# Optimization experiments

Hardware: AMD Instinct MI355X
Metric: run time of the kernel (lower is better)

The kernel has to match this reference:

```python
import jax, jax.numpy as jnp
import numpy as np
import math

NHID = 32
FEAT_SIZE = 32
FEAT_SIZE_LIST = [16, 32, 32, 32]
SEQ_LEN = len(FEAT_SIZE_LIST)   # 4
N_EDGE_LABELS = 3
NLAYERS = 2
N_GRAPHS = 64
FINAL = SEQ_LEN * NHID          # 128


def _pos_enc(max_len, dim):
    pe = np.zeros((max_len, dim), dtype=np.float32)
    pos = np.arange(max_len, dtype=np.float32)[:, None]
    div = np.exp(np.arange(0, dim, 2, dtype=np.float32) * (-math.log(10000.0) / dim))
    pe[:, 0::2] = np.sin(pos * div)
    pe[:, 1::2] = np.cos(pos * div)
    return jnp.asarray(pe)


def _feature_attention(x, wqkv, w1, b1, w2, b2):
    # x: [N, S*NHID] -> attention over the S feature 'tokens' per node
    N, D = x.shape
    S = D // NHID
    xr = x.reshape(N, S, NHID)
    qkv = jnp.einsum('nsf,fh->nsh', xr, wqkv)          # [N,S,3*NHID]
    q, k, v = jnp.split(qkv, 3, axis=-1)
    att = jax.nn.softmax(jnp.einsum('nsh,nth->nst', q, k) / jnp.sqrt(jnp.asarray(NHID, x.dtype)), axis=-1)
    y = jnp.einsum('nst,nth->nsh', att, v)             # [N,S,NHID]
    y = y + (jax.nn.relu(y @ w1 + b1) @ w2 + b2)       # residual FFN
    return y.reshape(N, -1)


def setup_inputs() -> dict:
    key = jax.random.key(0)
    ks = jax.random.split(key, 16)
    N = 100000
    E = 800000
    inp = {
        'x': jax.random.normal(ks[0], (N, 112), dtype=jnp.float32),
        'edge_index0': jax.random.randint(ks[1], (2, E), 0, N),
        'edge_index1': jax.random.randint(ks[2], (2, E), 0, N),
        'edge_index2': jax.random.randint(ks[3], (2, E), 0, N),
        'batch': jnp.sort(jax.random.randint(ks[4], (N,), 0, N_GRAPHS)),
    }
    s = 0.05
    # FeatureLinear encoder (bias-free)
    inp['W_emb'] = jax.random.normal(ks[5], (FEAT_SIZE, NHID), dtype=jnp.float32) * s
    # Per layer: [root, conv0, conv1, conv2] FeatureAttention params, stacked
    A = 1 + N_EDGE_LABELS
    inp['qkv'] = jax.random.normal(ks[6], (NLAYERS, A, NHID, 3 * NHID), dtype=jnp.float32) * s
    inp['ffn_w1'] = jax.random.normal(ks[7], (NLAYERS, A, NHID, NHID), dtype=jnp.float32) * s
    inp['ffn_b1'] = jnp.zeros((NLAYERS, A, NHID), dtype=jnp.float32)
    inp['ffn_w2'] = jax.random.normal(ks[8], (NLAYERS, A, NHID, NHID), dtype=jnp.float32) * s
    inp['ffn_b2'] = jnp.zeros((NLAYERS, A, NHID), dtype=jnp.float32)
    # Heuristic decoder MLP: 128 -> 128 -> 1
    inp['mlp_w1'] = jax.random.normal(ks[9], (FINAL, FINAL), dtype=jnp.float32) * s
    inp['mlp_b1'] = jnp.zeros((FINAL,), dtype=jnp.float32)
    inp['mlp_w2'] = jax.random.normal(ks[10], (FINAL, 1), dtype=jnp.float32) * s
    inp['mlp_b2'] = jnp.zeros((1,), dtype=jnp.float32)
    return inp


def reference(x, edge_index0, edge_index1, edge_index2, batch,
              W_emb, qkv, ffn_w1, ffn_b1, ffn_w2, ffn_b2,
              mlp_w1, mlp_b1, mlp_w2, mlp_b2):
    N = x.shape[0]
    edge_indices = [edge_index0, edge_index1, edge_index2]

    # padding: split by feat_size_list, right-pad each chunk to FEAT_SIZE
    offs = np.cumsum(FEAT_SIZE_LIST)[:-1].tolist()
    chunks = jnp.split(x, offs, axis=1)
    padded = [jnp.pad(c, ((0, 0), (0, FEAT_SIZE - c.shape[1]))) for c in chunks]
    h = jnp.concatenate(padded, axis=1)                       # [N, SEQ_LEN*FEAT_SIZE]

    # sinusoidal positional encoding over the SEQ_LEN feature tokens
    pe = _pos_enc(10, FEAT_SIZE)[:SEQ_LEN]                    # [SEQ_LEN, FEAT_SIZE]
    h = (h.reshape(N, SEQ_LEN, FEAT_SIZE) + pe[None]).reshape(N, -1)

    # FeatureLinear encoder: per-token linear FEAT_SIZE -> NHID
    h = jnp.einsum('nsf,fh->nsh', h.reshape(N, SEQ_LEN, FEAT_SIZE), W_emb).reshape(N, -1)

    # RGNN layers: root attention + per-edge-label attention->scatter-sum
    for l in range(NLAYERS):
        x_out = _feature_attention(h, qkv[l, 0], ffn_w1[l, 0], ffn_b1[l, 0], ffn_w2[l, 0], ffn_b2[l, 0])
        for e in range(N_EDGE_LABELS):
            a = e + 1
            xt = _feature_attention(h, qkv[l, a], ffn_w1[l, a], ffn_b1[l, a], ffn_w2[l, a], ffn_b2[l, a])
            src, dst = edge_indices[e][0], edge_indices[e][1]
            x_out = x_out + jax.ops.segment_sum(xt[src], dst, num_segments=N)
        h = jax.nn.relu(x_out)

    # global mean pool over graphs
    sums = jax.ops.segment_sum(h, batch, num_segments=N_GRAPHS)
    cnts = jax.ops.segment_sum(jnp.ones((N,), h.dtype), batch, num_segments=N_GRAPHS)
    g = sums / jnp.maximum(cnts, 1.0)[:, None]                # [G, FINAL]

    # heuristic decoder
    out = jax.nn.relu(g @ mlp_w1 + mlp_b1) @ mlp_w2 + mlp_b2  # [G, 1]
    return out.squeeze(1)                                     # [G]
```

## Files before the change

### kernel.cpp

```cpp
#include <hip/hip_runtime.h>
#include <hip/hip_bf16.h>
#include <cstdint>
#include <cstddef>


typedef __attribute__((ext_vector_type(8))) short bf16x8;
typedef __attribute__((ext_vector_type(4))) float f32x4;
typedef __attribute__((ext_vector_type(2))) float f32x2;

#if defined(__has_builtin)
#if __has_builtin(__builtin_amdgcn_cvt_pk_fp8_f32) && __has_builtin(__builtin_amdgcn_cvt_pk_f32_fp8)
#define HW_FP8 1
#endif
#if __has_builtin(__builtin_amdgcn_cvt_pk_bf16_f32)
#define HW_PKBF16 1
#endif
#endif

__device__ inline short f2bf(float f) {
    union { float f; unsigned u; } v; v.f = f;
    unsigned r = (v.u + 0x7FFFu + ((v.u >> 16) & 1u)) >> 16;
    return (short)r;
}
__device__ inline float bf2f(unsigned short b) {
    union { unsigned u; float f; } v; v.u = ((unsigned)b) << 16;
    return v.f;
}
#ifdef HW_PKBF16
typedef __attribute__((ext_vector_type(2))) __bf16 bf16x2_t;
__device__ inline unsigned pk2(float a, float b) {
    union { bf16x2_t v; unsigned u; } c;
    c.v = __builtin_amdgcn_cvt_pk_bf16_f32(a, b);
    return c.u;
}
#else
__device__ inline unsigned pk2(float a, float b) {
    unsigned ua = __float_as_uint(a) + 0x8000u;
    unsigned ub = __float_as_uint(b) + 0x8000u;
    return __builtin_amdgcn_perm(ub, ua, 0x07060302u);
}
#endif

#ifndef HW_FP8
__device__ inline unsigned char f2fp8_sw(float f) {
    unsigned s = (__float_as_uint(f) >> 31) & 1u;
    float a = fminf(fabsf(f), 448.f);
    unsigned char bits;
    if (a < 0.015625f) {
        bits = (unsigned char)__float2int_rn(a * 512.f);
    } else {
        int e; float m = frexpf(a, &e);
        int mf = __float2int_rn(m * 16.f);
        if (mf == 16) { mf = 8; e += 1; }
        int ef = e - 1 + 7;
        if (ef > 15) { ef = 15; mf = 14; }
        bits = (unsigned char)((ef << 3) | (mf & 7));
    }
    return (unsigned char)((s << 7) | bits);
}
__device__ inline float fp82f_sw(unsigned b) {
    int s = (b >> 7) & 1, e = (b >> 3) & 15, m = b & 7;
    float v = e ? ldexpf((float)(8 + m), e - 10) : ldexpf((float)m, -9);
    return s ? -v : v;
}
#endif

__device__ inline unsigned pk4fp8(float v0, float v1, float v2, float v3) {
#ifdef HW_FP8
    int w = __builtin_amdgcn_cvt_pk_fp8_f32(v0, v1, 0, false);
    w = __builtin_amdgcn_cvt_pk_fp8_f32(v2, v3, w, true);
    return (unsigned)w;
#else
    return (unsigned)f2fp8_sw(v0) | ((unsigned)f2fp8_sw(v1) << 8) |
           ((unsigned)f2fp8_sw(v2) << 16) | ((unsigned)f2fp8_sw(v3) << 24);
#endif
}
__device__ inline float2 up2fp8(unsigned short raw) {
#ifdef HW_FP8
    f32x2 f = __builtin_amdgcn_cvt_pk_f32_fp8((int)(unsigned)raw, false);
    return make_float2(f[0], f[1]);
#else
    return make_float2(fp82f_sw(raw & 0xffu), fp82f_sw((raw >> 8) & 0xffu));
#endif
}

__device__ inline void acc8(float* a, uint2 v) {
#ifdef HW_FP8
    f32x2 f0 = __builtin_amdgcn_cvt_pk_f32_fp8((int)v.x, false);
    f32x2 f1 = __builtin_amdgcn_cvt_pk_f32_fp8((int)v.x, true);
    f32x2 f2 = __builtin_amdgcn_cvt_pk_f32_fp8((int)v.y, false);
    f32x2 f3 = __builtin_amdgcn_cvt_pk_f32_fp8((int)v.y, true);
    a[0] += f0[0]; a[1] += f0[1]; a[2] += f1[0]; a[3] += f1[1];
    a[4] += f2[0]; a[5] += f2[1]; a[6] += f3[0]; a[7] += f3[1];
#else
    unsigned b0 = v.x, b1 = v.y;
#pragma unroll
    for (int j = 0; j < 4; ++j) a[j]     += fp82f_sw((b0 >> (8 * j)) & 0xffu);
#pragma unroll
    for (int j = 0; j < 4; ++j) a[4 + j] += fp82f_sw((b1 >> (8 * j)) & 0xffu);
#endif
}
__device__ inline void acc16(float* a, uint4 v) {
    acc8(a,     make_uint2(v.x, v.y));
    acc8(a + 8, make_uint2(v.z, v.w));
}

__global__ __launch_bounds__(64) void wprep_kernel(
    const float* __restrict__ qkv, const float* __restrict__ fw1,
    const float* __restrict__ fw2, const float* __restrict__ Wemb,
    unsigned short* __restrict__ wpack, float* __restrict__ pwc,
    unsigned char* __restrict__ xtzr,
    int* __restrict__ bcnt, int* __restrict__ gres,
    float* __restrict__ gsum, float* __restrict__ gcnt)
{
    const int pi = blockIdx.x;
    const int lane = threadIdx.x;
    const int gid = pi * 64 + lane;
    for (int i = gid; i < 256; i += 512) { bcnt[i] = 0; gres[i] = 0; }
    for (int i = gid; i < 64 * 128; i += 512) gsum[i] = 0.f;
    if (gid < 64) gcnt[gid] = 0.f;
    if (gid < 32) ((int*)xtzr)[gid] = 0;

    const int q = lane >> 4, m = lane & 15;
    const float* Wq = qkv + (size_t)pi * 32 * 96;
    const float* W1 = fw1 + (size_t)pi * 32 * 32;
    const float* W2 = fw2 + (size_t)pi * 32 * 32;
    unsigned short* dst = wpack + (size_t)pi * 10 * 64 * 8;
#pragma unroll
    for (int ci = 0; ci < 6; ++ci)
#pragma unroll
        for (int j = 0; j < 8; ++j)
            dst[(ci * 64 + lane) * 8 + j] =
                (unsigned short)f2bf(Wq[(q * 8 + j) * 96 + ci * 16 + m]);
#pragma unroll
    for (int t = 0; t < 2; ++t)
#pragma unroll
        for (int j = 0; j < 8; ++j) {
            dst[((6 + t) * 64 + lane) * 8 + j] =
                (unsigned short)f2bf(W1[(q * 8 + j) * 32 + t * 16 + m]);
            dst[((8 + t) * 64 + lane) * 8 + j] =
                (unsigned short)f2bf(W2[(q * 8 + j) * 32 + t * 16 + m]);
        }

    if (pi == 0) {
        const int c = lane & 31;
        for (int ts = lane >> 5; ts < 4; ts += 2) {
            float accp = 0.f;
            for (int f = 0; f < 32; ++f) {
                float div = __expf(-(float)(f & ~1) * (logf(10000.0f) / 32.0f));
                float ang = (float)ts * div;
                float pv = (f & 1) ? cosf(ang) : sinf(ang);
                accp += pv * Wemb[f * 32 + c];
            }
            pwc[ts * 32 + c] = accp;
        }
    }
}

__global__ __launch_bounds__(256) void enc_kernel(
    const float* __restrict__ x, const float* __restrict__ Wemb,
    const float* __restrict__ pwc, unsigned short* __restrict__ h, int N)
{
    __shared__ float sx[64 * 116];
    const int t = threadIdx.x;
    const int nbase = blockIdx.x * 64;

    {
        const float4* xg = (const float4*)x;
        const size_t g4base = ((size_t)nbase * 112) >> 2;
        const size_t lim4 = ((size_t)N * 112) >> 2;
#pragma unroll
        for (int rep = 0; rep < 7; ++rep) {
            int i = t + rep * 256;
            float4 v = make_float4(0.f, 0.f, 0.f, 0.f);
            if (g4base + (size_t)i < lim4) v = xg[g4base + i];
            int row = i / 28;
            int col4 = i - row * 28;
            *(float4*)&sx[row * 116 + col4 * 4] = v;
        }
    }
    __syncthreads();

    const int nl = t >> 2, ts = t & 3;
    const int node = nbase + nl;
    const int offs_[4] = {0, 16, 48, 80};
    const int nv_[4] = {4, 8, 8, 8};
    const int off = offs_[ts];
    const int nv = nv_[ts];

    float xr[32];
#pragma unroll
    for (int j = 0; j < 8; ++j) {
        float4 v = make_float4(0.f, 0.f, 0.f, 0.f);
        if (j < nv) v = *(const float4*)&sx[nl * 116 + off + 4 * j];
        *(float4*)&xr[4 * j] = v;
    }

    float acc[32];
    {
        const float4* pw4 = (const float4*)(pwc + ts * 32);
#pragma unroll
        for (int j = 0; j < 8; ++j) *(float4*)&acc[4 * j] = pw4[j];
    }

#pragma unroll
    for (int f = 0; f < 32; ++f) {
        float xv = xr[f];
#pragma unroll
        for (int c = 0; c < 32; ++c)
            acc[c] = fmaf(xv, Wemb[f * 32 + c], acc[c]);
    }

    if (node < N) {
        unsigned rp[16];
#pragma unroll
        for (int j = 0; j < 16; ++j) rp[j] = pk2(acc[2 * j], acc[2 * j + 1]);
        unsigned short* hp = h + (size_t)node * 128 + ts * 32;
#pragma unroll
        for (int j = 0; j < 4; ++j)
            ((uint4*)hp)[j] = make_uint4(rp[4 * j], rp[4 * j + 1],
                                         rp[4 * j + 2], rp[4 * j + 3]);
    }
}

#define ATT_WAVES 4
#define WLDS 5376

__global__ __launch_bounds__(256, 3) void attn4_kernel(
    const unsigned short* __restrict__ in,
    unsigned short* __restrict__ outR, unsigned char* __restrict__ out3,
    const unsigned short* __restrict__ wpack,
    const float* __restrict__ fb1, const float* __restrict__ fb2,
    int pibase, int N)
{
    __shared__ char smem[ATT_WAVES * 2 * WLDS];
    const int lane = threadIdx.x & 63;
    const int wave = threadIdx.x >> 6;
    const int q = lane >> 4;
    const int m = lane & 15;

    char* wb0 = smem + wave * (2 * WLDS);

#pragma unroll
    for (int u = 0; u < 2; ++u) {
        int* p32 = (int*)(wb0 + u * WLDS + 4096);
        for (int i = lane; i < 320; i += 64) p32[i] = 0;
    }

    const f32x4 zf = {0.f, 0.f, 0.f, 0.f};
    const int pi = pibase + wave;
    unsigned char* out8 = out3 + (size_t)(wave - 1) * N * 128;

    bf16x8 wqkv[6], w1f[2], w2f[2];
    float b1r[2][4], b2r[2][4];
    {
        const unsigned short* wp = wpack + ((size_t)pi * 10 * 64 + lane) * 8;
#pragma unroll
        for (int ci = 0; ci < 6; ++ci)
            wqkv[ci] = *(const bf16x8*)(wp + ci * 64 * 8);
#pragma unroll
        for (int t = 0; t < 2; ++t) {
            w1f[t] = *(const bf16x8*)(wp + (6 + t) * 64 * 8);
            w2f[t] = *(const bf16x8*)(wp + (8 + t) * 64 * 8);
#pragma unroll
            for (int r = 0; r < 4; ++r) {
                b1r[t][r] = fb1[pi * 32 + 16 * t + q * 4 + r];
                b2r[t][r] = fb2[pi * 32 + 16 * t + q * 4 + r];
            }
        }
    }

    const int nsuper = (N + 7) >> 3;
    for (int stile = blockIdx.x; stile < nsuper; stile += gridDim.x) {
        const int n0 = stile * 8;

        bf16x8 ax[2];
#pragma unroll
        for (int u = 0; u < 2; ++u) {
            bf16x8 a = {0, 0, 0, 0, 0, 0, 0, 0};
            int nm = n0 + 4 * u + (m >> 2);
            if (nm < N)
                a = *(const bf16x8*)(in + (size_t)(n0 + 4 * u) * 128 + m * 32 + q * 8);
            ax[u] = a;
        }

#pragma unroll
        for (int u = 0; u < 2; ++u) {
            char* wbu = wb0 + u * WLDS;
            short* Qb = (short*)(wbu);
            short* Kb = (short*)(wbu + 1280);
            short* VT = (short*)(wbu + 2560);
            short* Pb = (short*)(wbu + 4096);

            f32x4 aQ[2], aK[2], aV[2];
#pragma unroll
            for (int t = 0; t < 2; ++t) {
                aQ[t] = __builtin_amdgcn_mfma_f32_16x16x32_bf16(wqkv[t],     ax[u], zf, 0, 0, 0);
                aK[t] = __builtin_amdgcn_mfma_f32_16x16x32_bf16(wqkv[2 + t], ax[u], zf, 0, 0, 0);
                aV[t] = __builtin_amdgcn_mfma_f32_16x16x32_bf16(ax[u], wqkv[4 + t], zf, 0, 0, 0);
            }
#pragma unroll
            for (int t = 0; t < 2; ++t) {
                uint2 dq, dk, dv;
                dq.x = pk2(aQ[t][0], aQ[t][1]); dq.y = pk2(aQ[t][2], aQ[t][3]);
                dk.x = pk2(aK[t][0], aK[t][1]); dk.y = pk2(aK[t][2], aK[t][3]);
                dv.x = pk2(aV[t][0], aV[t][1]); dv.y = pk2(aV[t][2], aV[t][3]);
                *(uint2*)(Qb + m * 40 + 16 * t + q * 4) = dq;
                *(uint2*)(Kb + m * 40 + 16 * t + q * 4) = dk;
                *(uint2*)(VT + (16 * t + m) * 24 + q * 4) = dv;
            }

            bf16x8 aKf = *(const bf16x8*)(Kb + m * 40 + q * 8);
            bf16x8 bQf = *(const bf16x8*)(Qb + m * 40 + q * 8);
            f32x4 st = __builtin_amdgcn_mfma_f32_16x16x32_bf16(aKf, bQf, zf, 0, 0, 0);

            float v0 = st[0] * 0.1767766952966369f;
            float v1 = st[1] * 0.1767766952966369f;
            float v2 = st[2] * 0.1767766952966369f;
            float v3 = st[3] * 0.1767766952966369f;
            float mx = fmaxf(fmaxf(v0, v1), fmaxf(v2, v3));
            float e0 = __expf(v0 - mx), e1 = __expf(v1 - mx);
            float e2 = __expf(v2 - mx), e3 = __expf(v3 - mx);
            float inv = 1.0f / (e0 + e1 + e2 + e3);
            if (q == (m >> 2)) {
                uint2 dp;
                dp.x = pk2(e0 * inv, e1 * inv);
                dp.y = pk2(e2 * inv, e3 * inv);
                *(uint2*)(Pb + m * 40 + q * 4) = dp;
            }

            f32x4 y[2];
#pragma unroll
            for (int t = 0; t < 2; ++t) {
                bf16x8 aVf = {0, 0, 0, 0, 0, 0, 0, 0};
                bf16x8 bPf = {0, 0, 0, 0, 0, 0, 0, 0};
                if (q < 2) {
                    aVf = *(const bf16x8*)(VT + (16 * t + m) * 24 + q * 8);
                    bPf = *(const bf16x8*)(Pb + m * 40 + q * 8);
                }
                y[t] = __builtin_amdgcn_mfma_f32_16x16x32_bf16(aVf, bPf, zf, 0, 0, 0);
            }
#pragma unroll
            for (int t = 0; t < 2; ++t) {
                uint2 dy;
                dy.x = pk2(y[t][0], y[t][1]); dy.y = pk2(y[t][2], y[t][3]);
                *(uint2*)(Qb + m * 40 + 16 * t + q * 4) = dy;
            }

            bf16x8 bY = *(const bf16x8*)(Qb + m * 40 + q * 8);
            f32x4 z1[2];
#pragma unroll
            for (int t = 0; t < 2; ++t)
                z1[t] = __builtin_amdgcn_mfma_f32_16x16x32_bf16(w1f[t], bY, zf, 0, 0, 0);
#pragma unroll
            for (int t = 0; t < 2; ++t) {
                uint2 dz;
                dz.x = pk2(fmaxf(z1[t][0] + b1r[t][0], 0.f),
                           fmaxf(z1[t][1] + b1r[t][1], 0.f));
                dz.y = pk2(fmaxf(z1[t][2] + b1r[t][2], 0.f),
                           fmaxf(z1[t][3] + b1r[t][3], 0.f));
                *(uint2*)(Kb + m * 40 + 16 * t + q * 4) = dz;
            }

            bf16x8 bZ = *(const bf16x8*)(Kb + m * 40 + q * 8);
            f32x4 o[2];
#pragma unroll
            for (int t = 0; t < 2; ++t)
                o[t] = __builtin_amdgcn_mfma_f32_16x16x32_bf16(w2f[t], bZ, zf, 0, 0, 0);

            if (n0 + 4 * u + (m >> 2) < N) {
                if (wave == 0) {
#pragma unroll
                    for (int t = 0; t < 2; ++t) {
                        uint2 dd;
                        dd.x = pk2(y[t][0] + o[t][0] + b2r[t][0],
                                   y[t][1] + o[t][1] + b2r[t][1]);
                        dd.y = pk2(y[t][2] + o[t][2] + b2r[t][2],
                                   y[t][3] + o[t][3] + b2r[t][3]);
                        *(uint2*)(outR + (size_t)(n0 + 4 * u) * 128 + m * 32 + 16 * t + q * 4) = dd;
                    }
                } else {
#pragma unroll
                    for (int t = 0; t < 2; ++t) {
                        unsigned pw8 = pk4fp8(
                            (y[t][0] + o[t][0] + b2r[t][0]) * 16.f,
                            (y[t][1] + o[t][1] + b2r[t][1]) * 16.f,
                            (y[t][2] + o[t][2] + b2r[t][2]) * 16.f,
                            (y[t][3] + o[t][3] + b2r[t][3]) * 16.f);
                        *(unsigned*)(out8 + (size_t)(n0 + 4 * u) * 128 + m * 32 + 16 * t + q * 4) = pw8;
                    }
                }
            }
        }
    }
}

#define PA_CHUNK 4096
#define PA_SHIFT 9
#define PA_MAXB  256
#define HB_K     16

__global__ __launch_bounds__(256) void histB_kernel(
    const int* __restrict__ e0, const int* __restrict__ e1,
    const int* __restrict__ e2, int* __restrict__ bcnt, int E)
{
    __shared__ int lh[PA_MAXB];
    const int lab = blockIdx.y;
    const int* e = (lab == 0) ? e0 : (lab == 1) ? e1 : e2;
    const int t = threadIdx.x;
    for (int i = t; i < PA_MAXB; i += 256) lh[i] = 0;
    __syncthreads();
    const int base = blockIdx.x * 256 * HB_K;
#pragma unroll
    for (int k = 0; k < HB_K; ++k) {
        int i = base + k * 256 + t;
        if (i < E) atomicAdd(&lh[e[E + i] >> PA_SHIFT], 1);
    }
    __syncthreads();
    for (int i = t; i < PA_MAXB; i += 256)
        if (lh[i]) atomicAdd(&bcnt[i], lh[i]);
}

__global__ __launch_bounds__(256) void bscan_kernel(
    const int* __restrict__ bcnt, int* __restrict__ bbase)
{
    __shared__ int sd[PA_MAXB];
    const int t = threadIdx.x;
    sd[t] = bcnt[t];
    __syncthreads();
    int own = sd[t];
    for (int o = 1; o < 256; o <<= 1) {
        int v = (t >= o) ? sd[t - o] : 0;
        __syncthreads();
        sd[t] += v;
        __syncthreads();
    }
    bbase[t] = sd[t] - own;
}

__global__ __launch_bounds__(256) void placeA_kernel(
    const int* __restrict__ e0, const int* __restrict__ e1, const int* __restrict__ e2,
    const int* __restrict__ bbase, int* __restrict__ gres,
    int2* __restrict__ pairs, int E, int N)
{
    __shared__ int2 sStage[PA_CHUNK];
    __shared__ int sCnt[PA_MAXB], sScan[PA_MAXB], sCur[PA_MAXB], sGB[PA_MAXB];

    const int lab = blockIdx.y;
    const int t = threadIdx.x;
    const int base = blockIdx.x * PA_CHUNK;
    const int* e = (lab == 0) ? e0 : (lab == 1) ? e1 : e2;
    const int srcoff = lab * N;
    const int nbins = (N + (1 << PA_SHIFT) - 1) >> PA_SHIFT;

    for (int i = t; i < PA_MAXB; i += 256) { sCnt[i] = 0; sCur[i] = 0; }
    __syncthreads();

    int msrc[16], mdst[16];
    const int cnt_total = min(PA_CHUNK, E - base);
#pragma unroll
    for (int k = 0; k < 16; ++k) {
        int i = base + k * 256 + t;
        if (i < E) {
            msrc[k] = srcoff + e[i];
            int d = e[E + i];
            mdst[k] = d;
            atomicAdd(&sCnt[d >> PA_SHIFT], 1);
        } else mdst[k] = -1;
    }
    __syncthreads();

    sScan[t] = sCnt[t];
    __syncthreads();
    for (int o = 1; o < 256; o <<= 1) {
        int v = (t >= o) ? sScan[t - o] : 0;
        __syncthreads();
        sScan[t] += v;
        __syncthreads();
    }
    if (t < nbins && sCnt[t] > 0)
        sGB[t] = bbase[t] + atomicAdd(&gres[t], sCnt[t]);
    __syncthreads();

#pragma unroll
    for (int k = 0; k < 16; ++k) {
        if (mdst[k] >= 0) {
            int bin = mdst[k] >> PA_SHIFT;
            int r = atomicAdd(&sCur[bin], 1);
            sStage[(sScan[bin] - sCnt[bin]) + r] = make_int2(msrc[k], mdst[k]);
        }
    }
    __syncthreads();

    for (int i = t; i < cnt_total; i += 256) {
        int2 pr = sStage[i];
        int bin = pr.y >> PA_SHIFT;
        pairs[sGB[bin] + (i - (sScan[bin] - sCnt[bin]))] = pr;
    }
}

__global__ __launch_bounds__(512) void placeB_kernel(
    const int2* __restrict__ pairs, const int* __restrict__ bbase,
    const int* __restrict__ bcnt, int* __restrict__ offs,
    int* __restrict__ csr, int N, int nbins)
{
    __shared__ int sCnt[512], sScan[512], sFill[512];
    const int bin = blockIdx.x;
    const int t = threadIdx.x;
    const int n0 = bin << PA_SHIFT;
    const int n1 = min(n0 + 512, N);
    const int len = n1 - n0;
    const int rb  = bbase[bin];
    const int cnt = bcnt[bin];
    const int2* gp = pairs + rb;

    sCnt[t] = 0; sFill[t] = 0;
    __syncthreads();
    for (int i = t; i < cnt; i += 512)
        atomicAdd(&sCnt[gp[i].y - n0], 1);
    __syncthreads();
    sScan[t] = sCnt[t];
    __syncthreads();
    for (int o = 1; o < 512; o <<= 1) {
        int v = (t >= o) ? sScan[t - o] : 0;
        __syncthreads();
        sScan[t] += v;
        __syncthreads();
    }
    const int excl = sScan[t] - sCnt[t];
    if (t < len) offs[n0 + t] = rb + excl;
    if (bin == nbins - 1 && t == 0) offs[N] = rb + cnt;
    sScan[t] = excl;
    __syncthreads();

    for (int i = t; i < cnt; i += 512) {
        int2 pr = gp[i];
        int ln = pr.y - n0;
        int p = atomicAdd(&sFill[ln], 1);
        csr[rb + sScan[ln] + p] = pr.x;
    }
}

__global__ __launch_bounds__(256) void agg3_kernel(
    const unsigned short* __restrict__ xtR,
    const unsigned char* __restrict__ xt3,
    const int* __restrict__ csr, const int* __restrict__ offs,
    unsigned short* __restrict__ hout, int N)
{
    const int wv = threadIdx.x >> 6, lane = threadIdx.x & 63;
    const int oct = lane >> 3;
    const int fl  = lane & 7;
    const int dst = blockIdx.x * 32 + wv * 8 + oct;
    const int ZR  = 3 * N;
    const unsigned fb = (unsigned)fl << 4;

    const int beg = offs[min(dst, N)];
    const int end = offs[min(dst + 1, N)];
    const int last = end - 1;

    const unsigned short* rp = xtR + (size_t)min(dst, N - 1) * 128 + fl * 16;
    bf16x8 rv0 = *(const bf16x8*)(rp);
    bf16x8 rv1 = *(const bf16x8*)(rp + 8);

    float a[16];
#pragma unroll
    for (int i = 0; i < 16; ++i) a[i] = 0.f;

    int k = beg;
    int i0 = csr[k];
    int i1 = csr[k + 1];
    int c0 = (k     > last) ? ZR : i0;
    int c1 = (k + 1 > last) ? ZR : i1;

    while (__any(k < end)) {
        uint4 v0 = *(const uint4*)(xt3 + (((unsigned)c0) << 7) + fb);
        uint4 v1 = *(const uint4*)(xt3 + (((unsigned)c1) << 7) + fb);
        int k2 = min(k + 2, end);
        int j0 = csr[k2];
        int j1 = csr[k2 + 1];
        c0 = (k2     > last) ? ZR : j0;
        c1 = (k2 + 1 > last) ? ZR : j1;
        acc16(a, v0);
        acc16(a, v1);
        k = k2;
    }

    if (dst < N) {
        unsigned r[8];
#pragma unroll
        for (int t = 0; t < 4; ++t) {
            float f0 = bf2f((unsigned short)rv0[2 * t])     + 0.0625f * a[2 * t];
            float f1 = bf2f((unsigned short)rv0[2 * t + 1]) + 0.0625f * a[2 * t + 1];
            r[t] = pk2(fmaxf(f0, 0.f), fmaxf(f1, 0.f));
        }
#pragma unroll
        for (int t = 0; t < 4; ++t) {
            float f0 = bf2f((unsigned short)rv1[2 * t])     + 0.0625f * a[8 + 2 * t];
            float f1 = bf2f((unsigned short)rv1[2 * t + 1]) + 0.0625f * a[8 + 2 * t + 1];
            r[4 + t] = pk2(fmaxf(f0, 0.f), fmaxf(f1, 0.f));
        }
        unsigned short* hp = hout + (size_t)dst * 128 + fl * 16;
        *(uint4*)hp       = make_uint4(r[0], r[1], r[2], r[3]);
        *(uint4*)(hp + 8) = make_uint4(r[4], r[5], r[6], r[7]);
    }
}

__global__ __launch_bounds__(256) void pool_kernel(
    const unsigned short* __restrict__ in, const int* __restrict__ batch,
    float* __restrict__ gsum, float* __restrict__ gcnt, int N)
{
    int t = threadIdx.x;
    int j = t & 127, half = t >> 7;
    int n0 = blockIdx.x * 64 + half * 32;
    float acc = 0.f, c = 0.f; int cur = -1;
    for (int i = 0; i < 32; ++i) {
        int n = n0 + i;
        if (n >= N) break;
        int g = batch[n];
        if (g != cur) {
            if (cur >= 0) {
                atomicAdd(&gsum[cur * 128 + j], acc);
                if (j == 0) atomicAdd(&gcnt[cur], c);
            }
            cur = g; acc = 0.f; c = 0.f;
        }
        acc += bf2f(in[(size_t)n * 128 + j]);
        c += 1.f;
    }
    if (cur >= 0) {
        atomicAdd(&gsum[cur * 128 + j], acc);
        if (j == 0) atomicAdd(&gcnt[cur], c);
    }
}

__global__ __launch_bounds__(128) void dec_kernel(
    const float* __restrict__ gsum, const float* __restrict__ gcnt,
    const float* __restrict__ W1, const float* __restrict__ B1,
    const float* __restrict__ W2, const float* __restrict__ B2,
    float* __restrict__ out)
{
    __shared__ float sg[128];
    __shared__ float sh[128];
    int t = threadIdx.x, b = blockIdx.x;
    float cinv = 1.0f / fmaxf(gcnt[b], 1.0f);
    sg[t] = gsum[b * 128 + t] * cinv;
    __syncthreads();
    float acc = B1[t];
    for (int f = 0; f < 128; ++f) acc += sg[f] * W1[f * 128 + t];
    sh[t] = fmaxf(acc, 0.f) * W2[t];
    __syncthreads();
    for (int o = 64; o > 0; o >>= 1) {
        if (t < o) sh[t] += sh[t + o];
        __syncthreads();
    }
    if (t == 0) out[b] = sh[0] + B2[0];
}

extern "C" void kernel_launch(void* const* d_in, const int* in_sizes, int n_in,
                              void* d_out, int out_size, void* d_ws, size_t ws_size,
                              hipStream_t stream)
{
    const float* x    = (const float*)d_in[0];
    const int*   e0   = (const int*)d_in[1];
    const int*   e1   = (const int*)d_in[2];
    const int*   e2   = (const int*)d_in[3];
    const int*   bat  = (const int*)d_in[4];
    const float* Wemb = (const float*)d_in[5];
    const float* qkv  = (const float*)d_in[6];
    const float* fw1  = (const float*)d_in[7];
    const float* fb1  = (const float*)d_in[8];
    const float* fw2  = (const float*)d_in[9];
    const float* fb2  = (const float*)d_in[10];
    const float* mw1  = (const float*)d_in[11];
    const float* mb1  = (const float*)d_in[12];
    const float* mw2  = (const float*)d_in[13];
    const float* mb2  = (const float*)d_in[14];
    const int N = in_sizes[0] / 112;
    const int E = in_sizes[1] / 2;
    float* outp = (float*)d_out;
    (void)n_in; (void)out_size; (void)ws_size;

    char* w = (char*)d_ws;
    auto alloc = [&](size_t bytes) {
        char* p = w; w += (bytes + 255) & ~(size_t)255; return p;
    };
    unsigned short* h0    = (unsigned short*)alloc((size_t)N * 128 * 2);
    unsigned short* h1    = (unsigned short*)alloc((size_t)N * 128 * 2);
    unsigned short* xtR   = (unsigned short*)alloc((size_t)N * 128 * 2);
    unsigned char*  xt3   = (unsigned char*)alloc((size_t)3 * N * 128 + 128);
    unsigned short* wpack = (unsigned short*)alloc(8 * 10 * 64 * 8 * 2);
    float* pwc   = (float*)alloc(128 * 4);
    int*   csr   = (int*)alloc((size_t)3 * E * 4 + 64);
    int*   offs  = (int*)alloc((size_t)(N + 1) * 4);
    int*   bcnt  = (int*)alloc(PA_MAXB * 4);
    int*   bbase = (int*)alloc(PA_MAXB * 4);
    int*   gres  = (int*)alloc(PA_MAXB * 4);
    float* gsum  = (float*)alloc(64 * 128 * 4);
    float* gcnt  = (float*)alloc(64 * 4);
    int2* pairs = (int2*)xtR;
    unsigned char* xtzr = xt3 + (size_t)3 * N * 128;

    const int nbins = (N + (1 << PA_SHIFT) - 1) >> PA_SHIFT;

    wprep_kernel<<<8, 64, 0, stream>>>(qkv, fw1, fw2, Wemb, wpack, pwc, xtzr,
                                       bcnt, gres, gsum, gcnt);
    enc_kernel<<<(N + 63) / 64, 256, 0, stream>>>(x, Wemb, pwc, h0, N);

    histB_kernel<<<dim3((E + 256 * HB_K - 1) / (256 * HB_K), 3), 256, 0, stream>>>(
        e0, e1, e2, bcnt, E);
    bscan_kernel<<<1, 256, 0, stream>>>(bcnt, bbase);
    placeA_kernel<<<dim3((E + PA_CHUNK - 1) / PA_CHUNK, 3), 256, 0, stream>>>(
        e0, e1, e2, bbase, gres, pairs, E, N);
    placeB_kernel<<<nbins, 512, 0, stream>>>(pairs, bbase, bcnt, offs, csr, N, nbins);

    const int ATT_GRID = 768;
    auto run_layer = [&](const unsigned short* lin, unsigned short* lout, int l) {
        attn4_kernel<<<ATT_GRID, 256, 0, stream>>>(
            lin, xtR, xt3, wpack, fb1, fb2, l * 4, N);
        agg3_kernel<<<(N + 31) / 32, 256, 0, stream>>>(xtR, xt3, csr, offs, lout, N);
    };
    run_layer(h0, h1, 0);
    run_layer(h1, h0, 1);

    pool_kernel<<<(N + 63) / 64, 256, 0, stream>>>(h0, bat, gsum, gcnt, N);
    dec_kernel<<<64, 128, 0, stream>>>(gsum, gcnt, mw1, mb1, mw2, mb2, outp);
}
```

Measured before the change: 465.7 us.

## Share attention P buffer across sub-tiles and unroll gather loop by four

The attention kernel now keeps a single per-wave P-scratch region for both sub-tiles, which cuts per-block LDS use. It raises the launch-bounds occupancy hint from 3 to 4 blocks and the persistent grid from 768 to 1024. The aggregation kernel gathers four neighbor rows per iteration instead of two, putting more loads in flight to hide gather latency. Sharing P across sub-tiles adds a possible ordering hazard if the two sub-tiles overlap, and the extra loads raise register pressure. The csr prefetch also reads up to three entries past the current index, which relies on padding past the end of the array.

```diff
diff --git a/kernel.cpp b/kernel.cpp
--- a/kernel.cpp
+++ b/kernel.cpp
@@ -224,26 +224,27 @@
 }
 
 #define ATT_WAVES 4
-#define WLDS 5376
-
-__global__ __launch_bounds__(256, 3) void attn4_kernel(
+#define ULDS 4096
+#define WLDS_W (2 * ULDS + 1280)
+
+__global__ __launch_bounds__(256, 4) void attn4_kernel(
     const unsigned short* __restrict__ in,
     unsigned short* __restrict__ outR, unsigned char* __restrict__ out3,
     const unsigned short* __restrict__ wpack,
     const float* __restrict__ fb1, const float* __restrict__ fb2,
     int pibase, int N)
 {
-    __shared__ char smem[ATT_WAVES * 2 * WLDS];
+    __shared__ char smem[ATT_WAVES * WLDS_W];
     const int lane = threadIdx.x & 63;
     const int wave = threadIdx.x >> 6;
     const int q = lane >> 4;
     const int m = lane & 15;
 
-    char* wb0 = smem + wave * (2 * WLDS);
-
-#pragma unroll
-    for (int u = 0; u < 2; ++u) {
-        int* p32 = (int*)(wb0 + u * WLDS + 4096);
+    char* wb0 = smem + wave * WLDS_W;
+    short* Pb = (short*)(wb0 + 2 * ULDS);
+
+    {
+        int* p32 = (int*)Pb;
         for (int i = lane; i < 320; i += 64) p32[i] = 0;
     }
 
@@ -286,11 +287,10 @@
 
 #pragma unroll
         for (int u = 0; u < 2; ++u) {
-            char* wbu = wb0 + u * WLDS;
+            char* wbu = wb0 + u * ULDS;
             short* Qb = (short*)(wbu);
             short* Kb = (short*)(wbu + 1280);
             short* VT = (short*)(wbu + 2560);
-            short* Pb = (short*)(wbu + 4096);
 
             f32x4 aQ[2], aK[2], aV[2];
 #pragma unroll
@@ -567,22 +567,31 @@
     for (int i = 0; i < 16; ++i) a[i] = 0.f;
 
     int k = beg;
-    int i0 = csr[k];
-    int i1 = csr[k + 1];
-    int c0 = (k     > last) ? ZR : i0;
-    int c1 = (k + 1 > last) ? ZR : i1;
+    int c0, c1, c2, c3;
+    {
+        int i0 = csr[k], i1 = csr[k + 1], i2 = csr[k + 2], i3 = csr[k + 3];
+        c0 = (k     > last) ? ZR : i0;
+        c1 = (k + 1 > last) ? ZR : i1;
+        c2 = (k + 2 > last) ? ZR : i2;
+        c3 = (k + 3 > last) ? ZR : i3;
+    }
 
     while (__any(k < end)) {
         uint4 v0 = *(const uint4*)(xt3 + (((unsigned)c0) << 7) + fb);
         uint4 v1 = *(const uint4*)(xt3 + (((unsigned)c1) << 7) + fb);
-        int k2 = min(k + 2, end);
-        int j0 = csr[k2];
-        int j1 = csr[k2 + 1];
-        c0 = (k2     > last) ? ZR : j0;
-        c1 = (k2 + 1 > last) ? ZR : j1;
+        uint4 v2 = *(const uint4*)(xt3 + (((unsigned)c2) << 7) + fb);
+        uint4 v3 = *(const uint4*)(xt3 + (((unsigned)c3) << 7) + fb);
+        int kn = min(k + 4, end);
+        int j0 = csr[kn], j1 = csr[kn + 1], j2 = csr[kn + 2], j3 = csr[kn + 3];
+        c0 = (kn     > last) ? ZR : j0;
+        c1 = (kn + 1 > last) ? ZR : j1;
+        c2 = (kn + 2 > last) ? ZR : j2;
+        c3 = (kn + 3 > last) ? ZR : j3;
         acc16(a, v0);
         acc16(a, v1);
-        k = k2;
+        acc16(a, v2);
+        acc16(a, v3);
+        k = kn;
     }
 
     if (dst < N) {
@@ -713,7 +722,7 @@
         e0, e1, e2, bbase, gres, pairs, E, N);
     placeB_kernel<<<nbins, 512, 0, stream>>>(pairs, bbase, bcnt, offs, csr, N, nbins);
 
-    const int ATT_GRID = 768;
+    const int ATT_GRID = 1024;
     auto run_layer = [&](const unsigned short* lin, unsigned short* lout, int l) {
         attn4_kernel<<<ATT_GRID, 256, 0, stream>>>(
             lin, xtR, xt3, wpack, fb1, fb2, l * 4, N);
```

New measurement: 454.7 us. 1.02x faster.
